# Kernel tuning notes

Hardware: AMD Instinct MI355X
Metric: run time of the kernel (lower is better)

Reference implementation:

```python
import jax, jax.numpy as jnp
import numpy as np

EMBED = 1024
HEADS = 16
DK = EMBED // HEADS


def setup_inputs() -> dict:
    key = jax.random.key(0)
    ks = jax.random.split(key, 6)
    B, S = 2, 2048
    scale = 1.0 / np.sqrt(EMBED)
    x = jax.random.normal(ks[0], (B, S, EMBED), dtype=jnp.float32)
    Wq = jax.random.normal(ks[1], (EMBED, EMBED), dtype=jnp.float32) * scale
    Wk = jax.random.normal(ks[2], (EMBED, EMBED), dtype=jnp.float32) * scale
    Wv = jax.random.normal(ks[3], (EMBED, EMBED), dtype=jnp.float32) * scale
    Wo = jax.random.normal(ks[4], (EMBED, EMBED), dtype=jnp.float32) * scale
    qw = jnp.zeros((HEADS, 1), dtype=jnp.float32)  # quantum_weight, init quantum_scale=0
    return {"x": x, "Wq": Wq, "Wk": Wk, "Wv": Wv, "Wo": Wo, "qw": qw}


def reference(x, Wq, Wk, Wv, Wo, qw):
    B, S, E = x.shape
    # nn.Linear with no bias: y = x @ W.T; split heads -> [B,H,S,Dk]
    def proj(W):
        return (x @ W.T).reshape(B, S, HEADS, DK).transpose(0, 2, 1, 3)
    q, k, v = proj(Wq), proj(Wk), proj(Wv)
    scores = jnp.einsum('bhsd,bhtd->bhst', q, k) / np.sqrt(DK)
    attn = jax.nn.softmax(scores, axis=-1)  # dropout in eval mode: identity
    classical = jnp.einsum('bhst,bhtd->bhsd', attn, v)
    w = jax.nn.sigmoid(qw)[:, :, None]  # [H,1,1] per-head mixing weight
    out = w * jnp.sin(classical) + (1.0 - w) * classical
    out = out.transpose(0, 2, 1, 3).reshape(B, S, E)
    return out @ Wo.T
```

## Files before the change

### kernel.cpp

```cpp
#include <hip/hip_runtime.h>
#include <math.h>

constexpr int Ec  = 1024;
constexpr int Hc  = 16;
constexpr int DKc = 64;
constexpr int Bc  = 2;
constexpr int Sc  = 2048;
constexpr int Mc  = Bc * Sc;

typedef _Float16 half8 __attribute__((ext_vector_type(8)));
typedef _Float16 half4 __attribute__((ext_vector_type(4)));
typedef float    floatx4  __attribute__((ext_vector_type(4)));
typedef float    floatx16 __attribute__((ext_vector_type(16)));
typedef unsigned int uint2v __attribute__((ext_vector_type(2)));
typedef unsigned int uint4v __attribute__((ext_vector_type(4)));

#define MFMA16(a, b, c) __builtin_amdgcn_mfma_f32_16x16x32_f16(a, b, c, 0, 0, 0)
#define MFMA32(a, b, c) __builtin_amdgcn_mfma_f32_32x32x16_f16(a, b, c, 0, 0, 0)

__device__ __forceinline__ void async_lds16(const _Float16* g, _Float16* l)
{
    __builtin_amdgcn_global_load_lds(
        (const __attribute__((address_space(1))) unsigned int*)g,
        (__attribute__((address_space(3))) unsigned int*)l, 16, 0, 0);
}

__device__ __forceinline__ unsigned pkh2(float a, float b)
{
    return __builtin_bit_cast(unsigned, __builtin_amdgcn_cvt_pkrtz(a, b));
}

__global__ __launch_bounds__(256)
void convert_to_h(const float4* __restrict__ x,
                  const float4* __restrict__ wq,
                  const float4* __restrict__ wk,
                  const float4* __restrict__ wv,
                  const float4* __restrict__ wo,
                  half4* __restrict__ dst)
{
    const int i = blockIdx.x * 256 + threadIdx.x;
    const float4* src; int off;
    if      (i < 1048576) { src = x;  off = i; }
    else if (i < 1310720) { src = wq; off = i - 1048576; }
    else if (i < 1572864) { src = wk; off = i - 1310720; }
    else if (i < 1835008) { src = wv; off = i - 1572864; }
    else                  { src = wo; off = i - 1835008; }
    const float4 v = src[off];
    half4 o;
    o.x = (_Float16)v.x; o.y = (_Float16)v.y;
    o.z = (_Float16)v.z; o.w = (_Float16)v.w;
    dst[i] = o;
}

__device__ __forceinline__ void mfma_gemm_core64(const _Float16* __restrict__ A,
                                                 const _Float16* __restrict__ Bw,
                                                 int m0, int n0,
                                                 _Float16* As, _Float16* Bs,
                                                 floatx16 acc[2][2])
{
    const int tid  = threadIdx.x;
    const int wave = tid >> 6, lane = tid & 63;
    const int l31  = lane & 31, hi = lane >> 5;
    const int wrow = (wave >> 1) * 64, wcol = (wave & 1) * 64;

    const int srow8  = lane >> 3;
    const int schunk = (lane & 7) ^ (srow8 & 7);
    const _Float16* ga = A  + (size_t)(m0 + wave * 32 + srow8) * Ec + schunk * 8;
    const _Float16* gb = Bw + (size_t)(n0 + wave * 32 + srow8) * Ec + schunk * 8;
    _Float16* lA = As + (size_t)(wave * 32) * 64;
    _Float16* lB = Bs + (size_t)(wave * 32) * 64;

    for (int kt = 0; kt < Ec; kt += 64) {
#pragma unroll
        for (int c = 0; c < 4; ++c) {
            async_lds16(ga + (size_t)(c * 8) * Ec + kt, lA + c * 512);
            async_lds16(gb + (size_t)(c * 8) * Ec + kt, lB + c * 512);
        }
        __syncthreads();

        half8 af[2][4], bf[2][4];
#pragma unroll
        for (int f = 0; f < 2; ++f) {
            const int ra = wrow + f * 32 + l31;
            const int rb = wcol + f * 32 + l31;
#pragma unroll
            for (int ks = 0; ks < 4; ++ks) {
                const int sc = ((ks << 1) | hi);
                af[f][ks] = *(const half8*)&As[ra * 64 + ((sc ^ (ra & 7)) * 8)];
                bf[f][ks] = *(const half8*)&Bs[rb * 64 + ((sc ^ (rb & 7)) * 8)];
            }
        }
#pragma unroll
        for (int ks = 0; ks < 4; ++ks)
#pragma unroll
            for (int am = 0; am < 2; ++am)
#pragma unroll
                for (int bn = 0; bn < 2; ++bn)
                    acc[am][bn] = MFMA32(af[am][ks], bf[bn][ks], acc[am][bn]);
        __syncthreads();
    }
}

__global__ __launch_bounds__(256)
void gemm_qkv_fused(const _Float16* __restrict__ xh,
                    const _Float16* __restrict__ wall,
                    _Float16* __restrict__ Qh,
                    _Float16* __restrict__ Kh,
                    _Float16* __restrict__ VTh)
{
    __shared__ __align__(16) _Float16 As[128 * 64];
    __shared__ __align__(16) _Float16 Bs[128 * 64];
    const int lin = blockIdx.x;
    const int swz = (lin & 7) * 96 + (lin >> 3);
    const int m0  = (swz / 24) * 128;
    const int n0f = (swz % 24) * 128;

    floatx16 acc[2][2] = {};
    mfma_gemm_core64(xh, wall, m0, n0f, As, Bs, acc);

    const int tid  = threadIdx.x;
    const int wave = tid >> 6, lane = tid & 63;
    const int l31  = lane & 31, hi = lane >> 5;
    const int wrow = (wave >> 1) * 64, wcol = (wave & 1) * 64;

    const int z   = n0f >> 10;
    const int nl0 = n0f & 1023;

    if (z == 2) {
#pragma unroll
        for (int am = 0; am < 2; ++am)
#pragma unroll
            for (int bn = 0; bn < 2; ++bn) {
                const int n  = nl0 + wcol + bn * 32 + l31;
                const int hh = n >> 6, d = n & 63;
#pragma unroll
                for (int rq = 0; rq < 4; ++rq) {
                    const int mb = m0 + wrow + am * 32 + rq * 8 + hi * 4;
                    const int bb = mb >> 11, s = mb & (Sc - 1);
                    half4 pk;
#pragma unroll
                    for (int r = 0; r < 4; ++r)
                        pk[r] = (_Float16)acc[am][bn][rq * 4 + r];
                    *(half4*)&VTh[((size_t)((bb * Hc + hh) * DKc + d)) * Sc + s] = pk;
                }
            }
    } else {
        _Float16* out = (z == 0) ? Qh : Kh;
        const float scale = (z == 0) ? 0.18033688011112042f : 1.0f;
#pragma unroll
        for (int am = 0; am < 2; ++am)
#pragma unroll
            for (int bn = 0; bn < 2; ++bn) {
                const int n = nl0 + wcol + bn * 32 + l31;
#pragma unroll
                for (int r = 0; r < 16; ++r) {
                    const int m = m0 + wrow + am * 32
                                + (r & 3) + 8 * (r >> 2) + 4 * hi;
                    out[(size_t)m * Ec + n] = (_Float16)(acc[am][bn][r] * scale);
                }
            }
    }
}

__global__ __launch_bounds__(256)
void gemm_out_mfma(const _Float16* __restrict__ A,
                   const _Float16* __restrict__ W,
                   float* __restrict__ C)
{
    __shared__ __align__(16) _Float16 As[128 * 64];
    __shared__ __align__(16) _Float16 Bs[64 * 64];
    const int lin = blockIdx.x;
    const int swz = (lin & 7) * 64 + (lin >> 3);
    const int m0 = (swz >> 4) * 128, n0 = (swz & 15) * 64;

    const int tid  = threadIdx.x;
    const int wave = tid >> 6, lane = tid & 63;
    const int l31  = lane & 31, hi = lane >> 5;
    const int wrow = (wave >> 1) * 64, wcol = (wave & 1) * 32;

    const int srow8  = lane >> 3;
    const int schunk = (lane & 7) ^ (srow8 & 7);
    const _Float16* ga = A + (size_t)(m0 + wave * 32 + srow8) * Ec + schunk * 8;
    const _Float16* gb = W + (size_t)(n0 + wave * 16 + srow8) * Ec + schunk * 8;
    _Float16* lA = As + (size_t)(wave * 32) * 64;
    _Float16* lB = Bs + (size_t)(wave * 16) * 64;

    floatx16 acc[2] = {};

    for (int kt = 0; kt < Ec; kt += 64) {
#pragma unroll
        for (int c = 0; c < 4; ++c)
            async_lds16(ga + (size_t)(c * 8) * Ec + kt, lA + c * 512);
#pragma unroll
        for (int c = 0; c < 2; ++c)
            async_lds16(gb + (size_t)(c * 8) * Ec + kt, lB + c * 512);
        __syncthreads();

        half8 af[2][4], bf[4];
#pragma unroll
        for (int f = 0; f < 2; ++f) {
            const int ra = wrow + f * 32 + l31;
#pragma unroll
            for (int ks = 0; ks < 4; ++ks) {
                const int sc = ((ks << 1) | hi);
                af[f][ks] = *(const half8*)&As[ra * 64 + ((sc ^ (ra & 7)) * 8)];
            }
        }
        {
            const int rb = wcol + l31;
#pragma unroll
            for (int ks = 0; ks < 4; ++ks) {
                const int sc = ((ks << 1) | hi);
                bf[ks] = *(const half8*)&Bs[rb * 64 + ((sc ^ (rb & 7)) * 8)];
            }
        }
#pragma unroll
        for (int ks = 0; ks < 4; ++ks)
#pragma unroll
            for (int am = 0; am < 2; ++am)
                acc[am] = MFMA32(af[am][ks], bf[ks], acc[am]);
        __syncthreads();
    }

#pragma unroll
    for (int am = 0; am < 2; ++am) {
        const int n = n0 + wcol + l31;
#pragma unroll
        for (int r = 0; r < 16; ++r) {
            const int m = m0 + wrow + am * 32 + (r & 3) + 8 * (r >> 2) + 4 * hi;
            C[(size_t)m * Ec + n] = acc[am][r];
        }
    }
}

__global__ __launch_bounds__(256, 4)
void flash_attn(const _Float16* __restrict__ Qh,
                const _Float16* __restrict__ Kh,
                const _Float16* __restrict__ VTh,
                const float* __restrict__ qw,
                _Float16* __restrict__ Mixh)
{
    constexpr int BM = 128, BN = 64;
    constexpr int NT = Sc / BN;
    __shared__ __align__(16) _Float16 KV[2][2][64 * 64];

    const int tid  = threadIdx.x;
    const int wl   = tid >> 6;
    const int lane = tid & 63;
    const int l31  = lane & 31, hi = lane >> 5;

    const int lin = blockIdx.x;
    const int xcd = lin & 7, idx = lin >> 3;
    const int bh  = xcd * 4 + (idx >> 4);
    const int qx  = idx & 15;
    const int q0  = qx * BM;
    const int h   = bh & (Hc - 1), b = bh >> 4;

    half8 aq[4];
    {
        const _Float16* qp = Qh + (size_t)(b * Sc + q0 + wl * 32 + l31) * Ec
                                + h * DKc + hi * 8;
#pragma unroll
        for (int ks = 0; ks < 4; ++ks) aq[ks] = *(const half8*)(qp + ks * 16);
    }

    const int srow   = lane >> 3;
    const int schunk = (lane & 7) ^ srow;
    const _Float16* Kg = Kh + (size_t)(b * Sc + wl * 16 + srow) * Ec
                            + h * DKc + schunk * 8;
    const _Float16* Vg = VTh + ((size_t)(bh * DKc + wl * 16 + srow)) * Sc
                             + schunk * 8;

    const int xk = l31 & 7;
    const _Float16* kbase[4];
    const _Float16* vbase[4];
#pragma unroll
    for (int ks = 0; ks < 4; ++ks) {
        const int xo = ((((ks << 1) | hi) ^ xk) << 3);
        kbase[ks] = KV[0][0] + l31 * 64 + xo;
        vbase[ks] = KV[0][1] + l31 * 64 + xo;
    }
    _Float16* kd0 = KV[0][0] + (wl * 16) * 64;
    _Float16* vd0 = KV[0][1] + (wl * 16) * 64;

    floatx16 o[2] = {};
    float l_run = 0.f;

    async_lds16(Kg, kd0);
    async_lds16(Kg + (size_t)8 * Ec, kd0 + 512);
    async_lds16(Vg, vd0);
    async_lds16(Vg + (size_t)8 * Sc, vd0 + 512);
    __syncthreads();

    const _Float16* kgp = Kg + (size_t)BN * Ec;
    const _Float16* vgp = Vg + BN;

#define ATTN_TILE(CO)                                                         \
    {                                                                         \
        _Pragma("unroll")                                                     \
        for (int t = 0; t < 2; ++t) {                                         \
            floatx16 st = {};                                                 \
            _Pragma("unroll")                                                 \
            for (int ks = 0; ks < 4; ++ks)                                    \
                st = MFMA32(*(const half8*)(kbase[ks] + (CO) + t * 2048),     \
                            aq[ks], st);                                      \
            float p[16];                                                      \
            _Pragma("unroll")                                                 \
            for (int r = 0; r < 16; ++r) p[r] = __builtin_amdgcn_exp2f(st[r]);\
            float s8[8];                                                      \
            _Pragma("unroll")                                                 \
            for (int r = 0; r < 8; ++r) s8[r] = p[2 * r] + p[2 * r + 1];      \
            float s4[4];                                                      \
            _Pragma("unroll")                                                 \
            for (int r = 0; r < 4; ++r) s4[r] = s8[2 * r] + s8[2 * r + 1];    \
            l_run += ((s4[0] + s4[1]) + (s4[2] + s4[3]));                     \
            half8 pa[2];                                                      \
            _Pragma("unroll")                                                 \
            for (int e = 0; e < 2; ++e) {                                     \
                const unsigned X0 = pkh2(p[8 * e + 0], p[8 * e + 1]);         \
                const unsigned X1 = pkh2(p[8 * e + 2], p[8 * e + 3]);         \
                const unsigned Y0 = pkh2(p[8 * e + 4], p[8 * e + 5]);         \
                const unsigned Y1 = pkh2(p[8 * e + 6], p[8 * e + 7]);         \
                const uint2v s0 = __builtin_amdgcn_permlane32_swap(X0, Y0, false, false); \
                const uint2v s1 = __builtin_amdgcn_permlane32_swap(X1, Y1, false, false); \
                uint4v w; w.x = s0.x; w.y = s1.x; w.z = s0.y; w.w = s1.y;     \
                pa[e] = __builtin_bit_cast(half8, w);                         \
            }                                                                 \
            _Pragma("unroll")                                                 \
            for (int dt = 0; dt < 2; ++dt)                                    \
                _Pragma("unroll")                                             \
                for (int e = 0; e < 2; ++e) {                                 \
                    const half8 bv = *(const half8*)                          \
                        (vbase[2 * t + e] + (CO) + dt * 2048);                \
                    o[dt] = MFMA32(pa[e], bv, o[dt]);                         \
                }                                                             \
        }                                                                     \
    }

    for (int n = 0; n < NT; n += 2) {
        async_lds16(kgp, kd0 + 8192);
        async_lds16(kgp + (size_t)8 * Ec, kd0 + 8192 + 512);
        async_lds16(vgp, vd0 + 8192);
        async_lds16(vgp + (size_t)8 * Sc, vd0 + 8192 + 512);
        kgp += (size_t)BN * Ec; vgp += BN;

        ATTN_TILE(0)
        __syncthreads();

        if (n + 2 < NT) {
            async_lds16(kgp, kd0);
            async_lds16(kgp + (size_t)8 * Ec, kd0 + 512);
            async_lds16(vgp, vd0);
            async_lds16(vgp + (size_t)8 * Sc, vd0 + 512);
            kgp += (size_t)BN * Ec; vgp += BN;
        }

        ATTN_TILE(8192)
        __syncthreads();
    }
#undef ATTN_TILE

    l_run += __shfl_xor(l_run, 32);

    const float wmix = 1.f / (1.f + __expf(-qw[h]));
#pragma unroll
    for (int r = 0; r < 16; ++r) {
        const int row = (r & 3) + 8 * (r >> 2) + 4 * hi;
        const float inv = 1.f / __shfl(l_run, row);
        _Float16* mp = Mixh + (size_t)(b * Sc + q0 + wl * 32 + row) * Ec + h * DKc;
#pragma unroll
        for (int dt = 0; dt < 2; ++dt) {
            const float v = o[dt][r] * inv;
            mp[dt * 32 + l31] = (_Float16)(wmix * __sinf(v) + (1.f - wmix) * v);
        }
    }
}

extern "C" void kernel_launch(void* const* d_in, const int* in_sizes, int n_in,
                              void* d_out, int out_size, void* d_ws, size_t ws_size,
                              hipStream_t stream)
{
    const float* x  = (const float*)d_in[0];
    const float* Wq = (const float*)d_in[1];
    const float* Wk = (const float*)d_in[2];
    const float* Wv = (const float*)d_in[3];
    const float* Wo = (const float*)d_in[4];
    const float* qw = (const float*)d_in[5];
    float* out = (float*)d_out;

    _Float16* hb   = (_Float16*)d_ws;
    _Float16* xh   = hb;
    _Float16* wqh  = hb + (size_t)4 * 1024 * 1024;
    _Float16* woh  = hb + (size_t)7 * 1024 * 1024;
    _Float16* Qh   = hb + (size_t)8 * 1024 * 1024;
    _Float16* Kh   = hb + (size_t)12 * 1024 * 1024;
    _Float16* VTh  = hb + (size_t)16 * 1024 * 1024;
    _Float16* mixh = hb + (size_t)20 * 1024 * 1024;

    convert_to_h<<<dim3(8192), dim3(256), 0, stream>>>(
        (const float4*)x, (const float4*)Wq, (const float4*)Wk,
        (const float4*)Wv, (const float4*)Wo, (half4*)hb);

    gemm_qkv_fused<<<dim3(768), dim3(256), 0, stream>>>(
        xh, wqh, Qh, Kh, VTh);

    flash_attn<<<dim3(512), dim3(256), 0, stream>>>(
        Qh, Kh, VTh, qw, mixh);

    gemm_out_mfma<<<dim3(512), dim3(256), 0, stream>>>(
        mixh, woh, out);
}
```

Baseline: 188.7 us.

## Double-buffer LDS tiles in QKV and output GEMMs, remap blocks per XCD

Both projection GEMMs now keep two LDS buffers, so the async global-to-LDS load of the next K tile is issued before the MFMA work on the current tile and the two overlap. The block index mapping is also changed so each XCD gets a contiguous group of N tiles, which should improve L2 reuse of weight rows. This doubles LDS use per block, which can lower occupancy, and keeps one barrier per tile. The old shared GEMM core helper and the unused MFMA16 macro are removed.

```diff
diff --git a/kernel.cpp b/kernel.cpp
--- a/kernel.cpp
+++ b/kernel.cpp
@@ -15,7 +15,6 @@
 typedef unsigned int uint2v __attribute__((ext_vector_type(2)));
 typedef unsigned int uint4v __attribute__((ext_vector_type(4)));
 
-#define MFMA16(a, b, c) __builtin_amdgcn_mfma_f32_16x16x32_f16(a, b, c, 0, 0, 0)
 #define MFMA32(a, b, c) __builtin_amdgcn_mfma_f32_32x32x16_f16(a, b, c, 0, 0, 0)
 
 __device__ __forceinline__ void async_lds16(const _Float16* g, _Float16* l)
@@ -52,55 +51,6 @@
     dst[i] = o;
 }
 
-__device__ __forceinline__ void mfma_gemm_core64(const _Float16* __restrict__ A,
-                                                 const _Float16* __restrict__ Bw,
-                                                 int m0, int n0,
-                                                 _Float16* As, _Float16* Bs,
-                                                 floatx16 acc[2][2])
-{
-    const int tid  = threadIdx.x;
-    const int wave = tid >> 6, lane = tid & 63;
-    const int l31  = lane & 31, hi = lane >> 5;
-    const int wrow = (wave >> 1) * 64, wcol = (wave & 1) * 64;
-
-    const int srow8  = lane >> 3;
-    const int schunk = (lane & 7) ^ (srow8 & 7);
-    const _Float16* ga = A  + (size_t)(m0 + wave * 32 + srow8) * Ec + schunk * 8;
-    const _Float16* gb = Bw + (size_t)(n0 + wave * 32 + srow8) * Ec + schunk * 8;
-    _Float16* lA = As + (size_t)(wave * 32) * 64;
-    _Float16* lB = Bs + (size_t)(wave * 32) * 64;
-
-    for (int kt = 0; kt < Ec; kt += 64) {
-#pragma unroll
-        for (int c = 0; c < 4; ++c) {
-            async_lds16(ga + (size_t)(c * 8) * Ec + kt, lA + c * 512);
-            async_lds16(gb + (size_t)(c * 8) * Ec + kt, lB + c * 512);
-        }
-        __syncthreads();
-
-        half8 af[2][4], bf[2][4];
-#pragma unroll
-        for (int f = 0; f < 2; ++f) {
-            const int ra = wrow + f * 32 + l31;
-            const int rb = wcol + f * 32 + l31;
-#pragma unroll
-            for (int ks = 0; ks < 4; ++ks) {
-                const int sc = ((ks << 1) | hi);
-                af[f][ks] = *(const half8*)&As[ra * 64 + ((sc ^ (ra & 7)) * 8)];
-                bf[f][ks] = *(const half8*)&Bs[rb * 64 + ((sc ^ (rb & 7)) * 8)];
-            }
-        }
-#pragma unroll
-        for (int ks = 0; ks < 4; ++ks)
-#pragma unroll
-            for (int am = 0; am < 2; ++am)
-#pragma unroll
-                for (int bn = 0; bn < 2; ++bn)
-                    acc[am][bn] = MFMA32(af[am][ks], bf[bn][ks], acc[am][bn]);
-        __syncthreads();
-    }
-}
-
 __global__ __launch_bounds__(256)
 void gemm_qkv_fused(const _Float16* __restrict__ xh,
                     const _Float16* __restrict__ wall,
@@ -108,20 +58,68 @@
                     _Float16* __restrict__ Kh,
                     _Float16* __restrict__ VTh)
 {
-    __shared__ __align__(16) _Float16 As[128 * 64];
-    __shared__ __align__(16) _Float16 Bs[128 * 64];
+    __shared__ __align__(16) _Float16 As[2][128 * 64];
+    __shared__ __align__(16) _Float16 Bs[2][128 * 64];
+
     const int lin = blockIdx.x;
-    const int swz = (lin & 7) * 96 + (lin >> 3);
-    const int m0  = (swz / 24) * 128;
-    const int n0f = (swz % 24) * 128;
-
-    floatx16 acc[2][2] = {};
-    mfma_gemm_core64(xh, wall, m0, n0f, As, Bs, acc);
+    const int xcd = lin & 7, idx = lin >> 3;
+    const int nt  = xcd * 3 + idx % 3;
+    const int mt  = idx / 3;
+    const int m0  = mt * 128;
+    const int n0f = nt * 128;
 
     const int tid  = threadIdx.x;
     const int wave = tid >> 6, lane = tid & 63;
     const int l31  = lane & 31, hi = lane >> 5;
     const int wrow = (wave >> 1) * 64, wcol = (wave & 1) * 64;
+
+    const int srow8  = lane >> 3;
+    const int schunk = (lane & 7) ^ (srow8 & 7);
+    const _Float16* ga = xh   + (size_t)(m0  + wave * 32 + srow8) * Ec + schunk * 8;
+    const _Float16* gb = wall + (size_t)(n0f + wave * 32 + srow8) * Ec + schunk * 8;
+    const int lofs = (wave * 32) * 64;
+
+    floatx16 acc[2][2] = {};
+
+#define QKV_STAGE(b, kt)                                                      \
+    { _Pragma("unroll")                                                       \
+      for (int c = 0; c < 4; ++c) {                                           \
+          async_lds16(ga + (size_t)(c * 8) * Ec + (kt), &As[b][lofs + c * 512]); \
+          async_lds16(gb + (size_t)(c * 8) * Ec + (kt), &Bs[b][lofs + c * 512]); \
+      } }
+
+#define QKV_TILE(b)                                                           \
+    { half8 af[2][4], bf[2][4];                                               \
+      _Pragma("unroll")                                                       \
+      for (int f = 0; f < 2; ++f) {                                           \
+          const int ra = wrow + f * 32 + l31;                                 \
+          const int rb = wcol + f * 32 + l31;                                 \
+          _Pragma("unroll")                                                   \
+          for (int ks = 0; ks < 4; ++ks) {                                    \
+              const int sc = (ks << 1) | hi;                                  \
+              af[f][ks] = *(const half8*)&As[b][ra * 64 + ((sc ^ (ra & 7)) * 8)]; \
+              bf[f][ks] = *(const half8*)&Bs[b][rb * 64 + ((sc ^ (rb & 7)) * 8)]; \
+          } }                                                                 \
+      _Pragma("unroll")                                                       \
+      for (int ks = 0; ks < 4; ++ks)                                          \
+          _Pragma("unroll")                                                   \
+          for (int am = 0; am < 2; ++am)                                      \
+              _Pragma("unroll")                                               \
+              for (int bn = 0; bn < 2; ++bn)                                  \
+                  acc[am][bn] = MFMA32(af[am][ks], bf[bn][ks], acc[am][bn]); }
+
+    QKV_STAGE(0, 0)
+    __syncthreads();
+    for (int kt = 0; kt < Ec; kt += 128) {
+        QKV_STAGE(1, kt + 64)
+        QKV_TILE(0)
+        __syncthreads();
+        if (kt + 128 < Ec) QKV_STAGE(0, kt + 128)
+        QKV_TILE(1)
+        __syncthreads();
+    }
+#undef QKV_TILE
+#undef QKV_STAGE
 
     const int z   = n0f >> 10;
     const int nl0 = n0f & 1023;
@@ -167,11 +165,14 @@
                    const _Float16* __restrict__ W,
                    float* __restrict__ C)
 {
-    __shared__ __align__(16) _Float16 As[128 * 64];
-    __shared__ __align__(16) _Float16 Bs[64 * 64];
+    __shared__ __align__(16) _Float16 As[2][128 * 64];
+    __shared__ __align__(16) _Float16 Bs[2][64 * 64];
+
     const int lin = blockIdx.x;
-    const int swz = (lin & 7) * 64 + (lin >> 3);
-    const int m0 = (swz >> 4) * 128, n0 = (swz & 15) * 64;
+    const int xcd = lin & 7, idx = lin >> 3;
+    const int nt  = xcd * 2 + (idx & 1);
+    const int mt  = idx >> 1;
+    const int m0  = mt * 128, n0 = nt * 64;
 
     const int tid  = threadIdx.x;
     const int wave = tid >> 6, lane = tid & 63;
@@ -182,45 +183,53 @@
     const int schunk = (lane & 7) ^ (srow8 & 7);
     const _Float16* ga = A + (size_t)(m0 + wave * 32 + srow8) * Ec + schunk * 8;
     const _Float16* gb = W + (size_t)(n0 + wave * 16 + srow8) * Ec + schunk * 8;
-    _Float16* lA = As + (size_t)(wave * 32) * 64;
-    _Float16* lB = Bs + (size_t)(wave * 16) * 64;
+    const int lofsA = (wave * 32) * 64;
+    const int lofsB = (wave * 16) * 64;
 
     floatx16 acc[2] = {};
 
-    for (int kt = 0; kt < Ec; kt += 64) {
-#pragma unroll
-        for (int c = 0; c < 4; ++c)
-            async_lds16(ga + (size_t)(c * 8) * Ec + kt, lA + c * 512);
-#pragma unroll
-        for (int c = 0; c < 2; ++c)
-            async_lds16(gb + (size_t)(c * 8) * Ec + kt, lB + c * 512);
-        __syncthreads();
-
-        half8 af[2][4], bf[4];
-#pragma unroll
-        for (int f = 0; f < 2; ++f) {
-            const int ra = wrow + f * 32 + l31;
-#pragma unroll
-            for (int ks = 0; ks < 4; ++ks) {
-                const int sc = ((ks << 1) | hi);
-                af[f][ks] = *(const half8*)&As[ra * 64 + ((sc ^ (ra & 7)) * 8)];
-            }
-        }
-        {
-            const int rb = wcol + l31;
-#pragma unroll
-            for (int ks = 0; ks < 4; ++ks) {
-                const int sc = ((ks << 1) | hi);
-                bf[ks] = *(const half8*)&Bs[rb * 64 + ((sc ^ (rb & 7)) * 8)];
-            }
-        }
-#pragma unroll
-        for (int ks = 0; ks < 4; ++ks)
-#pragma unroll
-            for (int am = 0; am < 2; ++am)
-                acc[am] = MFMA32(af[am][ks], bf[ks], acc[am]);
-        __syncthreads();
-    }
+#define OUT_STAGE(b, kt)                                                      \
+    { _Pragma("unroll")                                                       \
+      for (int c = 0; c < 4; ++c)                                             \
+          async_lds16(ga + (size_t)(c * 8) * Ec + (kt), &As[b][lofsA + c * 512]); \
+      _Pragma("unroll")                                                       \
+      for (int c = 0; c < 2; ++c)                                             \
+          async_lds16(gb + (size_t)(c * 8) * Ec + (kt), &Bs[b][lofsB + c * 512]); }
+
+#define OUT_TILE(b)                                                           \
+    { half8 af[2][4], bf[4];                                                  \
+      _Pragma("unroll")                                                       \
+      for (int f = 0; f < 2; ++f) {                                           \
+          const int ra = wrow + f * 32 + l31;                                 \
+          _Pragma("unroll")                                                   \
+          for (int ks = 0; ks < 4; ++ks) {                                    \
+              const int sc = (ks << 1) | hi;                                  \
+              af[f][ks] = *(const half8*)&As[b][ra * 64 + ((sc ^ (ra & 7)) * 8)]; \
+          } }                                                                 \
+      { const int rb = wcol + l31;                                            \
+        _Pragma("unroll")                                                     \
+        for (int ks = 0; ks < 4; ++ks) {                                      \
+            const int sc = (ks << 1) | hi;                                    \
+            bf[ks] = *(const half8*)&Bs[b][rb * 64 + ((sc ^ (rb & 7)) * 8)];  \
+        } }                                                                   \
+      _Pragma("unroll")                                                       \
+      for (int ks = 0; ks < 4; ++ks)                                          \
+          _Pragma("unroll")                                                   \
+          for (int am = 0; am < 2; ++am)                                      \
+              acc[am] = MFMA32(af[am][ks], bf[ks], acc[am]); }
+
+    OUT_STAGE(0, 0)
+    __syncthreads();
+    for (int kt = 0; kt < Ec; kt += 128) {
+        OUT_STAGE(1, kt + 64)
+        OUT_TILE(0)
+        __syncthreads();
+        if (kt + 128 < Ec) OUT_STAGE(0, kt + 128)
+        OUT_TILE(1)
+        __syncthreads();
+    }
+#undef OUT_TILE
+#undef OUT_STAGE
 
 #pragma unroll
     for (int am = 0; am < 2; ++am) {
```

Measured after the change: 194.6 us. 3.1% more time.
